# Kernel tuning notes

Hardware: AMD Instinct MI355X
Metric: run time of the kernel (lower is better)

The kernel has to match this reference:

```python
import jax, jax.numpy as jnp
import numpy as np

N_NODES = 35
N_EDGES = 1190
N_VIEWS = 6
C1_IN, C1_OUT = 1, 256
C2_IN, C2_OUT = 256, 256
C3_IN, C3_OUT = 256, 64


def _nnconv(x, edge_attr, src, dst, nn_w, nn_b, lin_w, bias, c_in, c_out):
    """PyG NNConv with aggr='mean': per-edge MLP weight, gather-matvec-scatter."""
    # per-edge weight matrices: [E, c_in, c_out]
    W = jax.nn.relu(edge_attr @ nn_w.T + nn_b).reshape(-1, c_in, c_out)
    # gather source features and apply per-edge weight: [E, c_out]
    msg = jnp.einsum('ei,eio->eo', x[src], W)
    # scatter-mean into target nodes
    agg = jax.ops.segment_sum(msg, dst, num_segments=N_NODES)
    cnt = jax.ops.segment_sum(jnp.ones((msg.shape[0],), msg.dtype), dst,
                              num_segments=N_NODES)
    agg = agg / jnp.maximum(cnt, 1.0)[:, None]
    # root transform (lin has no bias in PyG) + conv bias
    return agg + x @ lin_w.T + bias


def setup_inputs() -> dict:
    key = jax.random.key(0)
    ks = jax.random.split(key, 16)
    s = 0.05
    x = jnp.ones((N_NODES, C1_IN), jnp.float32)
    edge_attr = jax.random.uniform(ks[0], (N_EDGES, N_VIEWS), jnp.float32)
    edge_index = jax.random.randint(ks[1], (2, N_EDGES), 0, N_NODES, jnp.int32)
    inp = {
        'x': x, 'edge_attr': edge_attr, 'edge_index': edge_index,
        'nn1_w': jax.random.normal(ks[2], (C1_IN * C1_OUT, N_VIEWS), jnp.float32) * s,
        'nn1_b': jax.random.normal(ks[3], (C1_IN * C1_OUT,), jnp.float32) * s,
        'lin1_w': jax.random.normal(ks[4], (C1_OUT, C1_IN), jnp.float32) * s,
        'b1': jax.random.normal(ks[5], (C1_OUT,), jnp.float32) * s,
        'nn2_w': jax.random.normal(ks[6], (C2_IN * C2_OUT, N_VIEWS), jnp.float32) * s,
        'nn2_b': jax.random.normal(ks[7], (C2_IN * C2_OUT,), jnp.float32) * s,
        'lin2_w': jax.random.normal(ks[8], (C2_OUT, C2_IN), jnp.float32) * s,
        'b2': jax.random.normal(ks[9], (C2_OUT,), jnp.float32) * s,
        'nn3_w': jax.random.normal(ks[10], (C3_IN * C3_OUT, N_VIEWS), jnp.float32) * s,
        'nn3_b': jax.random.normal(ks[11], (C3_IN * C3_OUT,), jnp.float32) * s,
        'lin3_w': jax.random.normal(ks[12], (C3_OUT, C3_IN), jnp.float32) * s,
        'b3': jax.random.normal(ks[13], (C3_OUT,), jnp.float32) * s,
    }
    return inp


def reference(x, edge_attr, edge_index, nn1_w, nn1_b, lin1_w, b1,
              nn2_w, nn2_b, lin2_w, b2, nn3_w, nn3_b, lin3_w, b3):
    src, dst = edge_index[0], edge_index[1]
    x = jax.nn.relu(_nnconv(x, edge_attr, src, dst, nn1_w, nn1_b, lin1_w, b1, C1_IN, C1_OUT))
    x = jax.nn.relu(_nnconv(x, edge_attr, src, dst, nn2_w, nn2_b, lin2_w, b2, C2_IN, C2_OUT))
    x = jax.nn.relu(_nnconv(x, edge_attr, src, dst, nn3_w, nn3_b, lin3_w, b3, C3_IN, C3_OUT))
    # CBT: pairwise L1 distances over feature dim -> [N, N]
    # (equivalent to repeat(35,1,1) / transpose / abs / sum since N == 35)
    cbt = jnp.abs(x[None, :, :] - x[:, None, :]).sum(-1)
    return cbt
```

## Files before the change

### kernel.cpp

```cpp
#include <hip/hip_runtime.h>


#define NN 35
#define NE 1190
#define TE 5

__global__ void zero_k(float* p, int n) {
    int t = blockIdx.x * 256 + threadIdx.x;
    if (t < n) p[t] = 0.f;
}

__global__ __launch_bounds__(256) void msg1_k(
    const float* __restrict__ x, const float* __restrict__ ea,
    const int* __restrict__ ei, const float* __restrict__ w1,
    const float* __restrict__ b1w, float* __restrict__ agg1,
    float* __restrict__ cnt) {
    int e = blockIdx.x;
    int o = threadIdx.x;
    int src = ei[e];
    int dst = ei[NE + e];
    float xs = x[src];
    const float* eap = ea + e * 6;
    const float* w = w1 + o * 6;
    float d = b1w[o];
#pragma unroll
    for (int v = 0; v < 6; v++) d = fmaf(eap[v], w[v], d);
    atomicAdd(agg1 + dst * 256 + o, xs * fmaxf(d, 0.f));
    if (o == 0) atomicAdd(cnt + dst, 1.0f);
}

__global__ __launch_bounds__(256) void x1_k(
    const float* __restrict__ x, const float* __restrict__ lin1,
    const float* __restrict__ b1, const float* __restrict__ agg1,
    const float* __restrict__ cnt, float* __restrict__ x1) {
    int n = blockIdx.x, o = threadIdx.x;
    float c = fmaxf(cnt[n], 1.f);
    float v = agg1[n * 256 + o] / c + x[n] * lin1[o] + b1[o];
    x1[n * 256 + o] = fmaxf(v, 0.f);
}

__global__ __launch_bounds__(512) void msg2_k(
    const float* __restrict__ x1, const float* __restrict__ ea,
    const int* __restrict__ ei, const float* __restrict__ w2,
    const float* __restrict__ b2w, float* __restrict__ agg2) {
    __shared__ float xs[TE][256];
    __shared__ float eas[TE][6];
    __shared__ int dsts[TE];
    __shared__ int srcs[TE];
    __shared__ float part[7][TE][64];
    int tid = threadIdx.x;
    int eg = blockIdx.x >> 2;
    int og = blockIdx.x & 3;
    int e0 = eg * TE;
    if (tid < TE) { dsts[tid] = ei[NE + e0 + tid]; srcs[tid] = ei[e0 + tid]; }
    if (tid >= 64 && tid < 64 + TE * 6) {
        int t = tid - 64;
        eas[t / 6][t % 6] = ea[e0 * 6 + t];
    }
    __syncthreads();
    for (int idx = tid; idx < TE * 256; idx += 512) {
        int te = idx >> 8, i = idx & 255;
        xs[te][i] = x1[srcs[te] * 256 + i];
    }
    __syncthreads();
    int ol = tid & 63;
    int o = og * 64 + ol;
    int ic = tid >> 6;
    float eareg[TE][6];
#pragma unroll
    for (int te = 0; te < TE; te++)
#pragma unroll
        for (int v = 0; v < 6; v++) eareg[te][v] = eas[te][v];
    float acc[TE] = {};
    for (int ii = 0; ii < 32; ii++) {
        int i = ic * 32 + ii;
        const float* w = w2 + (size_t)(i * 256 + o) * 6;
        float2 wa = *(const float2*)w;
        float2 wb = *(const float2*)(w + 2);
        float2 wc = *(const float2*)(w + 4);
        float b = b2w[i * 256 + o];
#pragma unroll
        for (int te = 0; te < TE; te++) {
            float d = b;
            d = fmaf(eareg[te][0], wa.x, d);
            d = fmaf(eareg[te][1], wa.y, d);
            d = fmaf(eareg[te][2], wb.x, d);
            d = fmaf(eareg[te][3], wb.y, d);
            d = fmaf(eareg[te][4], wc.x, d);
            d = fmaf(eareg[te][5], wc.y, d);
            acc[te] = fmaf(xs[te][i], fmaxf(d, 0.f), acc[te]);
        }
    }
    if (ic > 0) {
#pragma unroll
        for (int te = 0; te < TE; te++) part[ic - 1][te][ol] = acc[te];
    }
    __syncthreads();
    if (ic == 0) {
#pragma unroll
        for (int te = 0; te < TE; te++) {
            float s = acc[te];
#pragma unroll
            for (int p = 0; p < 7; p++) s += part[p][te][ol];
            atomicAdd(agg2 + dsts[te] * 256 + o, s);
        }
    }
}

__global__ __launch_bounds__(1024) void x2_k(
    const float* __restrict__ x1, const float* __restrict__ lin2,
    const float* __restrict__ b2, const float* __restrict__ agg2,
    const float* __restrict__ cnt, float* __restrict__ x2) {
    __shared__ float xr[256];
    __shared__ float part[3][256];
    int n = blockIdx.x, tid = threadIdx.x;
    int o = tid & 255, ic = tid >> 8;
    if (tid < 256) xr[tid] = x1[n * 256 + tid];
    __syncthreads();
    const float4* w = (const float4*)(lin2 + (size_t)o * 256 + ic * 64);
    float s = 0.f;
#pragma unroll
    for (int k = 0; k < 16; k++) {
        float4 wv = w[k];
        int i = ic * 64 + k * 4;
        s = fmaf(wv.x, xr[i], s);
        s = fmaf(wv.y, xr[i + 1], s);
        s = fmaf(wv.z, xr[i + 2], s);
        s = fmaf(wv.w, xr[i + 3], s);
    }
    if (ic > 0) part[ic - 1][o] = s;
    __syncthreads();
    if (ic == 0) {
        float tot = s + part[0][o] + part[1][o] + part[2][o];
        float c = fmaxf(cnt[n], 1.f);
        float v = agg2[n * 256 + o] / c + tot + b2[o];
        x2[n * 256 + o] = fmaxf(v, 0.f);
    }
}

__global__ __launch_bounds__(512) void msg3_k(
    const float* __restrict__ x2, const float* __restrict__ ea,
    const int* __restrict__ ei, const float* __restrict__ w3,
    const float* __restrict__ b3w, float* __restrict__ agg3) {
    __shared__ float xs[TE][128];
    __shared__ float eas[TE][6];
    __shared__ int dsts[TE];
    __shared__ int srcs[TE];
    __shared__ float part[7][TE][64];
    int tid = threadIdx.x;
    int eg = blockIdx.x >> 1;
    int ig = blockIdx.x & 1;
    int e0 = eg * TE;
    if (tid < TE) { dsts[tid] = ei[NE + e0 + tid]; srcs[tid] = ei[e0 + tid]; }
    if (tid >= 64 && tid < 64 + TE * 6) {
        int t = tid - 64;
        eas[t / 6][t % 6] = ea[e0 * 6 + t];
    }
    __syncthreads();
    for (int idx = tid; idx < TE * 128; idx += 512) {
        int te = idx >> 7, ii = idx & 127;
        xs[te][ii] = x2[srcs[te] * 256 + ig * 128 + ii];
    }
    __syncthreads();
    int ol = tid & 63;
    int ic = tid >> 6;
    float eareg[TE][6];
#pragma unroll
    for (int te = 0; te < TE; te++)
#pragma unroll
        for (int v = 0; v < 6; v++) eareg[te][v] = eas[te][v];
    float acc[TE] = {};
    for (int jj = 0; jj < 16; jj++) {
        int ii = ic * 16 + jj;
        int i = ig * 128 + ii;
        const float* w = w3 + (size_t)(i * 64 + ol) * 6;
        float2 wa = *(const float2*)w;
        float2 wb = *(const float2*)(w + 2);
        float2 wc = *(const float2*)(w + 4);
        float b = b3w[i * 64 + ol];
#pragma unroll
        for (int te = 0; te < TE; te++) {
            float d = b;
            d = fmaf(eareg[te][0], wa.x, d);
            d = fmaf(eareg[te][1], wa.y, d);
            d = fmaf(eareg[te][2], wb.x, d);
            d = fmaf(eareg[te][3], wb.y, d);
            d = fmaf(eareg[te][4], wc.x, d);
            d = fmaf(eareg[te][5], wc.y, d);
            acc[te] = fmaf(xs[te][ii], fmaxf(d, 0.f), acc[te]);
        }
    }
    if (ic > 0) {
#pragma unroll
        for (int te = 0; te < TE; te++) part[ic - 1][te][ol] = acc[te];
    }
    __syncthreads();
    if (ic == 0) {
#pragma unroll
        for (int te = 0; te < TE; te++) {
            float s = acc[te];
#pragma unroll
            for (int p = 0; p < 7; p++) s += part[p][te][ol];
            atomicAdd(agg3 + dsts[te] * 64 + ol, s);
        }
    }
}

__global__ __launch_bounds__(256) void x3_k(
    const float* __restrict__ x2, const float* __restrict__ lin3,
    const float* __restrict__ b3, const float* __restrict__ agg3,
    const float* __restrict__ cnt, float* __restrict__ x3) {
    __shared__ float xr[256];
    __shared__ float part[3][64];
    int n = blockIdx.x, tid = threadIdx.x;
    int o = tid & 63, ic = tid >> 6;
    xr[tid] = x2[n * 256 + tid];
    __syncthreads();
    const float4* w = (const float4*)(lin3 + (size_t)o * 256 + ic * 64);
    float s = 0.f;
#pragma unroll
    for (int k = 0; k < 16; k++) {
        float4 wv = w[k];
        int i = ic * 64 + k * 4;
        s = fmaf(wv.x, xr[i], s);
        s = fmaf(wv.y, xr[i + 1], s);
        s = fmaf(wv.z, xr[i + 2], s);
        s = fmaf(wv.w, xr[i + 3], s);
    }
    if (ic > 0) part[ic - 1][o] = s;
    __syncthreads();
    if (ic == 0) {
        float tot = s + part[0][o] + part[1][o] + part[2][o];
        float c = fmaxf(cnt[n], 1.f);
        x3[n * 64 + o] = fmaxf(agg3[n * 64 + o] / c + tot + b3[o], 0.f);
    }
}

__global__ __launch_bounds__(256) void cbt_k(const float* __restrict__ x3,
                                             float* __restrict__ out) {
    int t = blockIdx.x * 256 + threadIdx.x;
    if (t >= NN * NN) return;
    int i = t / NN, j = t % NN;
    const float* a = x3 + i * 64;
    const float* b = x3 + j * 64;
    float s = 0.f;
#pragma unroll
    for (int f = 0; f < 64; f++) s += fabsf(a[f] - b[f]);
    out[t] = s;
}

extern "C" void kernel_launch(void* const* d_in, const int* in_sizes, int n_in,
                              void* d_out, int out_size, void* d_ws, size_t ws_size,
                              hipStream_t stream) {
    const float* x    = (const float*)d_in[0];
    const float* ea   = (const float*)d_in[1];
    const int*   ei   = (const int*)d_in[2];
    const float* nn1w = (const float*)d_in[3];
    const float* nn1b = (const float*)d_in[4];
    const float* lin1 = (const float*)d_in[5];
    const float* b1   = (const float*)d_in[6];
    const float* nn2w = (const float*)d_in[7];
    const float* nn2b = (const float*)d_in[8];
    const float* lin2 = (const float*)d_in[9];
    const float* b2   = (const float*)d_in[10];
    const float* nn3w = (const float*)d_in[11];
    const float* nn3b = (const float*)d_in[12];
    const float* lin3 = (const float*)d_in[13];
    const float* b3   = (const float*)d_in[14];

    float* ws   = (float*)d_ws;
    float* x1   = ws;
    float* x2   = ws + 8960;
    float* x3v  = ws + 17920;
    float* agg1 = ws + 20160;
    float* agg2 = ws + 29120;
    float* agg3 = ws + 38080;
    float* cnt  = ws + 40320;
    float* out  = (float*)d_out;

    zero_k<<<(20195 + 255) / 256, 256, 0, stream>>>(agg1, 20195);
    msg1_k<<<NE, 256, 0, stream>>>(x, ea, ei, nn1w, nn1b, agg1, cnt);
    x1_k<<<NN, 256, 0, stream>>>(x, lin1, b1, agg1, cnt, x1);
    msg2_k<<<238 * 4, 512, 0, stream>>>(x1, ea, ei, nn2w, nn2b, agg2);
    x2_k<<<NN, 1024, 0, stream>>>(x1, lin2, b2, agg2, cnt, x2);
    msg3_k<<<238 * 2, 512, 0, stream>>>(x2, ea, ei, nn3w, nn3b, agg3);
    x3_k<<<NN, 256, 0, stream>>>(x2, lin3, b3, agg3, cnt, x3v);
    cbt_k<<<(NN * NN + 255) / 256, 256, 0, stream>>>(x3v, out);
}
```

Measured before the change: 147.0 us.

## Double edges per block in message kernels and fuse root transform with CBT

Doubles the edge tile in the layer-2 and layer-3 message kernels so each per-edge weight load is reused across ten edges. Layer 3 is re-split into four input-channel groups, and the source-feature staging uses float4 loads. Layer 1 now packs two edges per block, and the final root transform and pairwise L1 distance are fused into a single one-block kernel, removing a launch and a round trip through global memory. The trade-offs are more registers per thread and a serial single-block tail for the fused kernel.

```diff
diff --git a/kernel.cpp b/kernel.cpp
--- a/kernel.cpp
+++ b/kernel.cpp
@@ -3,20 +3,22 @@
 
 #define NN 35
 #define NE 1190
-#define TE 5
+#define TE 10
+#define NG 119
 
 __global__ void zero_k(float* p, int n) {
     int t = blockIdx.x * 256 + threadIdx.x;
     if (t < n) p[t] = 0.f;
 }
 
-__global__ __launch_bounds__(256) void msg1_k(
+__global__ __launch_bounds__(512) void msg1_k(
     const float* __restrict__ x, const float* __restrict__ ea,
     const int* __restrict__ ei, const float* __restrict__ w1,
     const float* __restrict__ b1w, float* __restrict__ agg1,
     float* __restrict__ cnt) {
-    int e = blockIdx.x;
-    int o = threadIdx.x;
+    int tid = threadIdx.x;
+    int e = blockIdx.x * 2 + (tid >> 8);
+    int o = tid & 255;
     int src = ei[e];
     int dst = ei[NE + e];
     float xs = x[src];
@@ -39,11 +41,11 @@
     x1[n * 256 + o] = fmaxf(v, 0.f);
 }
 
-__global__ __launch_bounds__(512) void msg2_k(
+__global__ __launch_bounds__(512, 4) void msg2_k(
     const float* __restrict__ x1, const float* __restrict__ ea,
     const int* __restrict__ ei, const float* __restrict__ w2,
     const float* __restrict__ b2w, float* __restrict__ agg2) {
-    __shared__ float xs[TE][256];
+    __shared__ __attribute__((aligned(16))) float xs[TE][256];
     __shared__ float eas[TE][6];
     __shared__ int dsts[TE];
     __shared__ int srcs[TE];
@@ -58,9 +60,9 @@
         eas[t / 6][t % 6] = ea[e0 * 6 + t];
     }
     __syncthreads();
-    for (int idx = tid; idx < TE * 256; idx += 512) {
-        int te = idx >> 8, i = idx & 255;
-        xs[te][i] = x1[srcs[te] * 256 + i];
+    for (int idx = tid; idx < TE * 64; idx += 512) {
+        int te = idx >> 6, q = idx & 63;
+        ((float4*)xs[te])[q] = ((const float4*)(x1 + srcs[te] * 256))[q];
     }
     __syncthreads();
     int ol = tid & 63;
@@ -80,15 +82,17 @@
         float2 wc = *(const float2*)(w + 4);
         float b = b2w[i * 256 + o];
 #pragma unroll
-        for (int te = 0; te < TE; te++) {
-            float d = b;
-            d = fmaf(eareg[te][0], wa.x, d);
-            d = fmaf(eareg[te][1], wa.y, d);
-            d = fmaf(eareg[te][2], wb.x, d);
-            d = fmaf(eareg[te][3], wb.y, d);
-            d = fmaf(eareg[te][4], wc.x, d);
-            d = fmaf(eareg[te][5], wc.y, d);
-            acc[te] = fmaf(xs[te][i], fmaxf(d, 0.f), acc[te]);
+        for (int te = 0; te < TE; te += 2) {
+            float dx = b, dy = b;
+            dx = fmaf(eareg[te][0], wa.x, dx); dy = fmaf(eareg[te + 1][0], wa.x, dy);
+            dx = fmaf(eareg[te][1], wa.y, dx); dy = fmaf(eareg[te + 1][1], wa.y, dy);
+            dx = fmaf(eareg[te][2], wb.x, dx); dy = fmaf(eareg[te + 1][2], wb.x, dy);
+            dx = fmaf(eareg[te][3], wb.y, dx); dy = fmaf(eareg[te + 1][3], wb.y, dy);
+            dx = fmaf(eareg[te][4], wc.x, dx); dy = fmaf(eareg[te + 1][4], wc.x, dy);
+            dx = fmaf(eareg[te][5], wc.y, dx); dy = fmaf(eareg[te + 1][5], wc.y, dy);
+            dx = fmaxf(dx, 0.f);               dy = fmaxf(dy, 0.f);
+            acc[te] = fmaf(xs[te][i], dx, acc[te]);
+            acc[te + 1] = fmaf(xs[te + 1][i], dy, acc[te + 1]);
         }
     }
     if (ic > 0) {
@@ -138,18 +142,18 @@
     }
 }
 
-__global__ __launch_bounds__(512) void msg3_k(
+__global__ __launch_bounds__(512, 4) void msg3_k(
     const float* __restrict__ x2, const float* __restrict__ ea,
     const int* __restrict__ ei, const float* __restrict__ w3,
     const float* __restrict__ b3w, float* __restrict__ agg3) {
-    __shared__ float xs[TE][128];
+    __shared__ __attribute__((aligned(16))) float xs[TE][64];
     __shared__ float eas[TE][6];
     __shared__ int dsts[TE];
     __shared__ int srcs[TE];
     __shared__ float part[7][TE][64];
     int tid = threadIdx.x;
-    int eg = blockIdx.x >> 1;
-    int ig = blockIdx.x & 1;
+    int eg = blockIdx.x >> 2;
+    int ig = blockIdx.x & 3;
     int e0 = eg * TE;
     if (tid < TE) { dsts[tid] = ei[NE + e0 + tid]; srcs[tid] = ei[e0 + tid]; }
     if (tid >= 64 && tid < 64 + TE * 6) {
@@ -157,9 +161,10 @@
         eas[t / 6][t % 6] = ea[e0 * 6 + t];
     }
     __syncthreads();
-    for (int idx = tid; idx < TE * 128; idx += 512) {
-        int te = idx >> 7, ii = idx & 127;
-        xs[te][ii] = x2[srcs[te] * 256 + ig * 128 + ii];
+    for (int idx = tid; idx < TE * 16; idx += 512) {
+        int te = idx >> 4, q = idx & 15;
+        ((float4*)xs[te])[q] =
+            ((const float4*)(x2 + srcs[te] * 256 + ig * 64))[q];
     }
     __syncthreads();
     int ol = tid & 63;
@@ -170,24 +175,26 @@
 #pragma unroll
         for (int v = 0; v < 6; v++) eareg[te][v] = eas[te][v];
     float acc[TE] = {};
-    for (int jj = 0; jj < 16; jj++) {
-        int ii = ic * 16 + jj;
-        int i = ig * 128 + ii;
+    for (int jj = 0; jj < 8; jj++) {
+        int ii = ic * 8 + jj;
+        int i = ig * 64 + ii;
         const float* w = w3 + (size_t)(i * 64 + ol) * 6;
         float2 wa = *(const float2*)w;
         float2 wb = *(const float2*)(w + 2);
         float2 wc = *(const float2*)(w + 4);
         float b = b3w[i * 64 + ol];
 #pragma unroll
-        for (int te = 0; te < TE; te++) {
-            float d = b;
-            d = fmaf(eareg[te][0], wa.x, d);
-            d = fmaf(eareg[te][1], wa.y, d);
-            d = fmaf(eareg[te][2], wb.x, d);
-            d = fmaf(eareg[te][3], wb.y, d);
-            d = fmaf(eareg[te][4], wc.x, d);
-            d = fmaf(eareg[te][5], wc.y, d);
-            acc[te] = fmaf(xs[te][ii], fmaxf(d, 0.f), acc[te]);
+        for (int te = 0; te < TE; te += 2) {
+            float dx = b, dy = b;
+            dx = fmaf(eareg[te][0], wa.x, dx); dy = fmaf(eareg[te + 1][0], wa.x, dy);
+            dx = fmaf(eareg[te][1], wa.y, dx); dy = fmaf(eareg[te + 1][1], wa.y, dy);
+            dx = fmaf(eareg[te][2], wb.x, dx); dy = fmaf(eareg[te + 1][2], wb.x, dy);
+            dx = fmaf(eareg[te][3], wb.y, dx); dy = fmaf(eareg[te + 1][3], wb.y, dy);
+            dx = fmaf(eareg[te][4], wc.x, dx); dy = fmaf(eareg[te + 1][4], wc.x, dy);
+            dx = fmaf(eareg[te][5], wc.y, dx); dy = fmaf(eareg[te + 1][5], wc.y, dy);
+            dx = fmaxf(dx, 0.f);               dy = fmaxf(dy, 0.f);
+            acc[te] = fmaf(xs[te][ii], dx, acc[te]);
+            acc[te + 1] = fmaf(xs[te + 1][ii], dy, acc[te + 1]);
         }
     }
     if (ic > 0) {
@@ -206,47 +213,46 @@
     }
 }
 
-__global__ __launch_bounds__(256) void x3_k(
+__global__ __launch_bounds__(1024) void x3cbt_k(
     const float* __restrict__ x2, const float* __restrict__ lin3,
     const float* __restrict__ b3, const float* __restrict__ agg3,
-    const float* __restrict__ cnt, float* __restrict__ x3) {
-    __shared__ float xr[256];
-    __shared__ float part[3][64];
-    int n = blockIdx.x, tid = threadIdx.x;
-    int o = tid & 63, ic = tid >> 6;
-    xr[tid] = x2[n * 256 + tid];
-    __syncthreads();
-    const float4* w = (const float4*)(lin3 + (size_t)o * 256 + ic * 64);
-    float s = 0.f;
-#pragma unroll
-    for (int k = 0; k < 16; k++) {
-        float4 wv = w[k];
-        int i = ic * 64 + k * 4;
-        s = fmaf(wv.x, xr[i], s);
-        s = fmaf(wv.y, xr[i + 1], s);
-        s = fmaf(wv.z, xr[i + 2], s);
-        s = fmaf(wv.w, xr[i + 3], s);
-    }
-    if (ic > 0) part[ic - 1][o] = s;
-    __syncthreads();
-    if (ic == 0) {
-        float tot = s + part[0][o] + part[1][o] + part[2][o];
+    const float* __restrict__ cnt, float* __restrict__ out) {
+    __shared__ float x2s[NN * 256];
+    __shared__ float x3s[NN * 65];
+    int tid = threadIdx.x;
+    for (int idx = tid; idx < NN * 256; idx += 1024) x2s[idx] = x2[idx];
+    __syncthreads();
+    for (int j = tid; j < NN * 64; j += 1024) {
+        int n = j >> 6, o = j & 63;
+        const float4* w = (const float4*)(lin3 + (size_t)o * 256);
+        const float* xr = x2s + n * 256;
+        float s0 = 0.f, s1 = 0.f;
+#pragma unroll 8
+        for (int k = 0; k < 64; k += 2) {
+            float4 wa = w[k], wb = w[k + 1];
+            int i = k * 4;
+            s0 = fmaf(wa.x, xr[i], s0);
+            s0 = fmaf(wa.y, xr[i + 1], s0);
+            s0 = fmaf(wa.z, xr[i + 2], s0);
+            s0 = fmaf(wa.w, xr[i + 3], s0);
+            s1 = fmaf(wb.x, xr[i + 4], s1);
+            s1 = fmaf(wb.y, xr[i + 5], s1);
+            s1 = fmaf(wb.z, xr[i + 6], s1);
+            s1 = fmaf(wb.w, xr[i + 7], s1);
+        }
         float c = fmaxf(cnt[n], 1.f);
-        x3[n * 64 + o] = fmaxf(agg3[n * 64 + o] / c + tot + b3[o], 0.f);
-    }
-}
-
-__global__ __launch_bounds__(256) void cbt_k(const float* __restrict__ x3,
-                                             float* __restrict__ out) {
-    int t = blockIdx.x * 256 + threadIdx.x;
-    if (t >= NN * NN) return;
-    int i = t / NN, j = t % NN;
-    const float* a = x3 + i * 64;
-    const float* b = x3 + j * 64;
-    float s = 0.f;
-#pragma unroll
-    for (int f = 0; f < 64; f++) s += fabsf(a[f] - b[f]);
-    out[t] = s;
+        x3s[n * 65 + o] = fmaxf(agg3[j] / c + s0 + s1 + b3[o], 0.f);
+    }
+    __syncthreads();
+    for (int p = tid; p < NN * NN; p += 1024) {
+        int i = p / NN, j = p % NN;
+        const float* a = x3s + i * 65;
+        const float* b = x3s + j * 65;
+        float s = 0.f;
+#pragma unroll
+        for (int f = 0; f < 64; f++) s += fabsf(a[f] - b[f]);
+        out[p] = s;
+    }
 }
 
 extern "C" void kernel_launch(void* const* d_in, const int* in_sizes, int n_in,
@@ -271,7 +277,6 @@
     float* ws   = (float*)d_ws;
     float* x1   = ws;
     float* x2   = ws + 8960;
-    float* x3v  = ws + 17920;
     float* agg1 = ws + 20160;
     float* agg2 = ws + 29120;
     float* agg3 = ws + 38080;
@@ -279,11 +284,10 @@
     float* out  = (float*)d_out;
 
     zero_k<<<(20195 + 255) / 256, 256, 0, stream>>>(agg1, 20195);
-    msg1_k<<<NE, 256, 0, stream>>>(x, ea, ei, nn1w, nn1b, agg1, cnt);
+    msg1_k<<<NE / 2, 512, 0, stream>>>(x, ea, ei, nn1w, nn1b, agg1, cnt);
     x1_k<<<NN, 256, 0, stream>>>(x, lin1, b1, agg1, cnt, x1);
-    msg2_k<<<238 * 4, 512, 0, stream>>>(x1, ea, ei, nn2w, nn2b, agg2);
+    msg2_k<<<NG * 4, 512, 0, stream>>>(x1, ea, ei, nn2w, nn2b, agg2);
     x2_k<<<NN, 1024, 0, stream>>>(x1, lin2, b2, agg2, cnt, x2);
-    msg3_k<<<238 * 2, 512, 0, stream>>>(x2, ea, ei, nn3w, nn3b, agg3);
-    x3_k<<<NN, 256, 0, stream>>>(x2, lin3, b3, agg3, cnt, x3v);
-    cbt_k<<<(NN * NN + 255) / 256, 256, 0, stream>>>(x3v, out);
-}
+    msg3_k<<<NG * 4, 512, 0, stream>>>(x2, ea, ei, nn3w, nn3b, agg3);
+    x3cbt_k<<<1, 1024, 0, stream>>>(x2, lin3, b3, agg3, cnt, out);
+}
```

After: 205.5 us. 39.8% more time.
